# Performance work log

Measured on AMD Instinct MI355X. Metric: run time of the kernel, lower is better.

The kernel has to match this reference:

```python
import jax, jax.numpy as jnp
import numpy as np

BS, SEQ, DK = 4, 4096, 128

def setup_inputs() -> dict:
    key = jax.random.key(0)
    kq, kk, kv = jax.random.split(key, 3)
    q = jax.random.normal(kq, (BS, SEQ, DK), dtype=jnp.float32)
    k = jax.random.normal(kk, (BS, SEQ, DK), dtype=jnp.float32)
    v = jax.random.normal(kv, (BS, SEQ, DK), dtype=jnp.float32)
    return {"q": q, "k": k, "v": v}

def reference(q, k, v):
    d_k = q.shape[-1]
    # scores: [bs, s_q, s_k]
    scaled = jnp.einsum('bqd,bkd->bqk', q, k) / jnp.sqrt(jnp.asarray(d_k, q.dtype))
    # NOTE: original torch code applies softmax over dim=1 (query axis), faithfully reproduced here.
    attn = jax.nn.softmax(scaled, axis=1)
    return jnp.einsum('bqk,bkd->bqd', attn, v)
```

## Files before the change

### kernel.cpp

```cpp
#include <hip/hip_runtime.h>
#include <hip/hip_bf16.h>

#define BS  4
#define SEQ 4096
#define DK  128

#define C1_SCALE (1.4426950408889634f / 11.313708498984761f)

typedef __attribute__((ext_vector_type(8))) short bf16x8;
typedef __attribute__((ext_vector_type(4))) float f32x4;
typedef unsigned short ushort_t;

__device__ inline unsigned pk_bf16(float a, float b) {
    __hip_bfloat162 h = __float22bfloat162_rn(make_float2(a, b));
    union { __hip_bfloat162 h2; unsigned u; } cv;
    cv.h2 = h;
    return cv.u;
}

__device__ inline bf16x8 pk8(float4 a, float4 b) {
    union { bf16x8 v; unsigned u[4]; } r;
    r.u[0] = pk_bf16(a.x, a.y);
    r.u[1] = pk_bf16(a.z, a.w);
    r.u[2] = pk_bf16(b.x, b.y);
    r.u[3] = pk_bf16(b.z, b.w);
    return r.v;
}

__device__ inline void gld_lds16(const ushort_t* g, ushort_t* l) {
    __builtin_amdgcn_global_load_lds(
        (const __attribute__((address_space(1))) unsigned int*)g,
        (__attribute__((address_space(3))) unsigned int*)l,
        16, 0, 0);
}

__global__ __launch_bounds__(256) void cast_qk_sw(
    const float* __restrict__ Q, const float* __restrict__ K,
    ushort_t* __restrict__ Qb, ushort_t* __restrict__ Kb)
{
    const int g = blockIdx.x * 256 + threadIdx.x;
    const int q = g >> 4, ap = g & 15;
    const int a = ap ^ (q & 15);
    const float* src = Q + (size_t)q * DK + a * 8;
    float4 x = *(const float4*)src, y = *(const float4*)(src + 4);
    x.x *= C1_SCALE; x.y *= C1_SCALE; x.z *= C1_SCALE; x.w *= C1_SCALE;
    y.x *= C1_SCALE; y.y *= C1_SCALE; y.z *= C1_SCALE; y.w *= C1_SCALE;
    *(bf16x8*)(Qb + (size_t)g * 8) = pk8(x, y);
    src = K + (size_t)q * DK + a * 8;
    float4 x2 = *(const float4*)src, y2 = *(const float4*)(src + 4);
    *(bf16x8*)(Kb + (size_t)g * 8) = pk8(x2, y2);
}

__global__ __launch_bounds__(256) void sdpa_lsum(
    const ushort_t* __restrict__ Qb, const ushort_t* __restrict__ Kb,
    float* __restrict__ lp)
{
    __shared__ ushort_t Qs[2][4096];

    const int kt = blockIdx.x, qs = blockIdx.y, b = blockIdx.z;
    const int tid = threadIdx.x;
    const int w = tid >> 6, lane = tid & 63, ln = lane & 15, quad = lane >> 4;

    bf16x8 ka[2][4];
#pragma unroll
    for (int mt = 0; mt < 2; ++mt)
#pragma unroll
        for (int c = 0; c < 4; ++c)
            ka[mt][c] = *(const bf16x8*)(Kb +
                ((size_t)(b * SEQ) + kt * 128 + w * 32 + mt * 16 + ln) * DK +
                (((c * 4 + quad) ^ ln) * 8));

    float ls[2][4] = {};
    const ushort_t* qtb = Qb + ((size_t)(b * SEQ + qs * 512)) * DK;

#define A_DMA(BUF, I)                                                          \
    {                                                                          \
        _Pragma("unroll")                                                      \
        for (int j = 0; j < 2; ++j)                                            \
            gld_lds16(qtb + (size_t)(I) * 4096 + (j * 256 + tid) * 8,          \
                      &Qs[BUF][(j * 256 + w * 64) * 8]);                       \
    }

#define A_CMP(BUF)                                                             \
    {                                                                          \
        bf16x8 qf[2][4];                                                       \
        _Pragma("unroll")                                                      \
        for (int nt = 0; nt < 2; ++nt)                                         \
            _Pragma("unroll")                                                  \
            for (int c = 0; c < 4; ++c)                                        \
                qf[nt][c] = *(const bf16x8*)&Qs[BUF][(nt * 16 + ln) * 128 +    \
                                    (((c * 4 + quad) ^ ln) * 8)];              \
        _Pragma("unroll")                                                      \
        for (int mt = 0; mt < 2; ++mt)                                         \
            _Pragma("unroll")                                                  \
            for (int nt = 0; nt < 2; ++nt) {                                   \
                f32x4 s = {0.f, 0.f, 0.f, 0.f};                                \
                __builtin_amdgcn_s_setprio(1);                                 \
                _Pragma("unroll")                                              \
                for (int c = 0; c < 4; ++c)                                    \
                    s = __builtin_amdgcn_mfma_f32_16x16x32_bf16(               \
                        ka[mt][c], qf[nt][c], s, 0, 0, 0);                     \
                __builtin_amdgcn_s_setprio(0);                                 \
                _Pragma("unroll")                                              \
                for (int r = 0; r < 4; ++r)                                    \
                    ls[mt][r] += __builtin_amdgcn_exp2f(s[r]);                 \
            }                                                                  \
    }

    A_DMA(0, 0)
    for (int ii = 0; ii < 8; ++ii) {
        const int i0 = 2 * ii;
        __syncthreads();
        A_DMA(1, i0 + 1)
        A_CMP(0)
        __syncthreads();
        if (ii < 7) A_DMA(0, i0 + 2)
        A_CMP(1)
    }
#undef A_DMA
#undef A_CMP

#pragma unroll
    for (int mt = 0; mt < 2; ++mt)
#pragma unroll
        for (int r = 0; r < 4; ++r) {
            float vv = ls[mt][r];
            vv += __shfl_xor(vv, 1);
            vv += __shfl_xor(vv, 2);
            vv += __shfl_xor(vv, 4);
            vv += __shfl_xor(vv, 8);
            ls[mt][r] = vv;
        }
    if (ln < 8) {
        int k = kt * 128 + w * 32 + (ln >> 2) * 16 + quad * 4 + (ln & 3);
        lp[((size_t)(qs * BS + b)) * SEQ + k] = ls[ln >> 2][ln & 3];
    }
}

__global__ __launch_bounds__(256) void vb_transpose(
    const float* __restrict__ V, const float* __restrict__ lp,
    ushort_t* __restrict__ VbT)
{
    __shared__ float Vl[64][132];
    __shared__ float Wl[64];

    const int kt = blockIdx.x, b = blockIdx.y;
    const int tid = threadIdx.x;
    const int k0 = kt * 64;
    {
        int r = tid >> 2, sg = tid & 3;
        const float* src = V + ((size_t)(b * SEQ) + k0 + r) * DK + sg * 32;
#pragma unroll
        for (int i = 0; i < 8; ++i)
            *(float4*)&Vl[r][sg * 32 + i * 4] = *(const float4*)(src + i * 4);
    }
    if (tid < 64) {
        float s = 0.f;
#pragma unroll
        for (int qs = 0; qs < 8; ++qs)
            s += lp[((size_t)(qs * BS + b)) * SEQ + k0 + tid];
        Wl[tid] = 1.0f / s;
    }
    __syncthreads();

    const int d = tid >> 1, kh = tid & 1;
    unsigned u[16];
#pragma unroll
    for (int j = 0; j < 16; ++j) {
        int row = kh * 32 + j * 2;
        u[j] = pk_bf16(Vl[row][d] * Wl[row], Vl[row + 1][d] * Wl[row + 1]);
    }
    ushort_t* dst = VbT + ((size_t)(b * DK) + d) * SEQ + k0 + kh * 32;
#pragma unroll
    for (int i = 0; i < 4; ++i) {
        uint4 t4; t4.x = u[i*4]; t4.y = u[i*4+1]; t4.z = u[i*4+2]; t4.w = u[i*4+3];
        *(uint4*)(dst + i * 8) = t4;
    }
}

__global__ __launch_bounds__(256) void sdpa_out(
    const ushort_t* __restrict__ Qb, const ushort_t* __restrict__ Kb,
    const ushort_t* __restrict__ VbT,
    float* __restrict__ Op, float* __restrict__ O, int use_partial)
{
    __shared__ ushort_t Kt[2][8192];
    __shared__ ushort_t Vt[2][8192];
    __shared__ ushort_t Pt[4096];

    const int g  = blockIdx.x;
    const int qt = blockIdx.y;
    const int ks = g >> 2, b = g & 3;
    const int tid = threadIdx.x;
    const int w = tid >> 6, lane = tid & 63, ln = lane & 15, quad = lane >> 4;

    bf16x8 qa[4][4];
#pragma unroll
    for (int nt = 0; nt < 4; ++nt)
#pragma unroll
        for (int c = 0; c < 4; ++c)
            qa[c][nt] = *(const bf16x8*)(Qb +
                ((size_t)(b * SEQ) + qt * 64 + nt * 16 + ln) * DK +
                (((c * 4 + quad) ^ ln) * 8));

    f32x4 acc[4][2];
#pragma unroll
    for (int i = 0; i < 4; ++i)
#pragma unroll
        for (int j = 0; j < 2; ++j) acc[i][j] = (f32x4){0.f, 0.f, 0.f, 0.f};

    const ushort_t* ksrc = Kb + ((size_t)(b * SEQ) + ks * 1024) * DK;
    const ushort_t* vsrc = VbT + ((size_t)(b * DK)) * SEQ + ks * 1024;
    const int vd = tid >> 3, vap = tid & 7;

#define O_DMA(BUF, PH)                                                         \
    {                                                                          \
        _Pragma("unroll")                                                      \
        for (int j = 0; j < 4; ++j)                                            \
            gld_lds16(ksrc + (size_t)(PH) * 64 * DK + (j * 256 + tid) * 8,     \
                      &Kt[BUF][(j * 256 + w * 64) * 8]);                       \
        _Pragma("unroll")                                                      \
        for (int j = 0; j < 4; ++j)                                            \
            gld_lds16(vsrc + (size_t)(j * 32 + vd) * SEQ + (PH) * 64 +         \
                          ((vap ^ (vd & 7)) * 8),                              \
                      &Vt[BUF][(j * 256 + w * 64) * 8]);                       \
    }

#define QK_PHASE(BUF)                                                          \
    {                                                                          \
        bf16x8 kf[4];                                                          \
        _Pragma("unroll")                                                      \
        for (int c = 0; c < 4; ++c)                                            \
            kf[c] = *(const bf16x8*)&Kt[BUF][(w * 16 + ln) * 128 +             \
                                             (((c * 4 + quad) ^ ln) * 8)];     \
        _Pragma("unroll")                                                      \
        for (int nt = 0; nt < 4; ++nt) {                                       \
            f32x4 s = {0.f, 0.f, 0.f, 0.f};                                    \
            __builtin_amdgcn_s_setprio(1);                                     \
            _Pragma("unroll")                                                  \
            for (int c = 0; c < 4; ++c)                                        \
                s = __builtin_amdgcn_mfma_f32_16x16x32_bf16(kf[c], qa[c][nt], s, 0, 0, 0); \
            __builtin_amdgcn_s_setprio(0);                                     \
            uint2 pw;                                                          \
            pw.x = pk_bf16(__builtin_amdgcn_exp2f(s[0]),                       \
                           __builtin_amdgcn_exp2f(s[1]));                      \
            pw.y = pk_bf16(__builtin_amdgcn_exp2f(s[2]),                       \
                           __builtin_amdgcn_exp2f(s[3]));                      \
            const int q = nt * 16 + ln;                                        \
            const int a16 = w * 2 + (quad >> 1);                               \
            *(uint2*)&Pt[q * 64 + ((a16 ^ (q & 7)) * 8) + (quad & 1) * 4] = pw; \
        }                                                                      \
    }

#define PV_PHASE(BUF)                                                          \
    {                                                                          \
        _Pragma("unroll")                                                      \
        for (int kc = 0; kc < 2; ++kc) {                                       \
            bf16x8 pa[4], vfr[2];                                              \
            _Pragma("unroll")                                                  \
            for (int qf2 = 0; qf2 < 4; ++qf2)                                  \
                pa[qf2] = *(const bf16x8*)&Pt[(qf2 * 16 + ln) * 64 +           \
                                    (((kc * 4 + quad) ^ (ln & 7)) * 8)];       \
            _Pragma("unroll")                                                  \
            for (int dt = 0; dt < 2; ++dt)                                     \
                vfr[dt] = *(const bf16x8*)&Vt[BUF][(w * 32 + dt * 16 + ln) * 64 + \
                                    (((kc * 4 + quad) ^ (ln & 7)) * 8)];       \
            __builtin_amdgcn_s_setprio(1);                                     \
            _Pragma("unroll")                                                  \
            for (int qf2 = 0; qf2 < 4; ++qf2)                                  \
                _Pragma("unroll")                                              \
                for (int dt = 0; dt < 2; ++dt)                                 \
                    acc[qf2][dt] = __builtin_amdgcn_mfma_f32_16x16x32_bf16(    \
                        pa[qf2], vfr[dt], acc[qf2][dt], 0, 0, 0);              \
            __builtin_amdgcn_s_setprio(0);                                     \
        }                                                                      \
    }

    O_DMA(0, 0)
    for (int ph = 0; ph < 16; ++ph) {
        const int cur = ph & 1;
        __syncthreads();
        if (ph < 15) O_DMA(cur ^ 1, ph + 1)
        QK_PHASE(cur)
        __syncthreads();
        PV_PHASE(cur)
    }
#undef O_DMA
#undef QK_PHASE
#undef PV_PHASE

    if (use_partial) {
        float* dst = Op + (size_t)ks * ((size_t)BS * SEQ * DK) +
                     ((size_t)(b * SEQ) + qt * 64 + quad * 4) * DK + w * 32 + ln;
#pragma unroll
        for (int qf2 = 0; qf2 < 4; ++qf2)
#pragma unroll
            for (int dt = 0; dt < 2; ++dt)
#pragma unroll
                for (int r = 0; r < 4; ++r)
                    dst[((size_t)(qf2 * 16 + r)) * DK + dt * 16] = acc[qf2][dt][r];
    } else {
#pragma unroll
        for (int qf2 = 0; qf2 < 4; ++qf2)
#pragma unroll
            for (int dt = 0; dt < 2; ++dt)
#pragma unroll
                for (int r = 0; r < 4; ++r)
                    atomicAdd(&O[((size_t)(b * SEQ) + qt * 64 + qf2 * 16 + quad * 4 + r) * DK +
                                 w * 32 + dt * 16 + ln], acc[qf2][dt][r]);
    }
}

__global__ __launch_bounds__(256) void reduce4(
    const float* __restrict__ Op, float* __restrict__ O)
{
    const size_t N = (size_t)BS * SEQ * DK;
    size_t i = ((size_t)blockIdx.x * 256 + threadIdx.x) * 4;
    float4 a0 = *(const float4*)(Op + i);
    float4 a1 = *(const float4*)(Op + N + i);
    float4 a2 = *(const float4*)(Op + 2 * N + i);
    float4 a3 = *(const float4*)(Op + 3 * N + i);
    float4 r;
    r.x = a0.x + a1.x + a2.x + a3.x;
    r.y = a0.y + a1.y + a2.y + a3.y;
    r.z = a0.z + a1.z + a2.z + a3.z;
    r.w = a0.w + a1.w + a2.w + a3.w;
    *(float4*)(O + i) = r;
}

extern "C" void kernel_launch(void* const* d_in, const int* in_sizes, int n_in,
                              void* d_out, int out_size, void* d_ws, size_t ws_size,
                              hipStream_t stream) {
    const float* q = (const float*)d_in[0];
    const float* k = (const float*)d_in[1];
    const float* v = (const float*)d_in[2];
    float* out = (float*)d_out;

    const size_t QKV = (size_t)BS * SEQ * DK;
    float*    lp  = (float*)d_ws;
    ushort_t* Qb  = (ushort_t*)((char*)d_ws + (1 << 20));
    ushort_t* Kb  = Qb + QKV;
    ushort_t* VbT = Kb + QKV;
    float*    Op  = (float*)(VbT + QKV);

    const size_t need_p = (1u << 20) + 3 * QKV * 2 + 4 * QKV * sizeof(float);

    cast_qk_sw<<<dim3(BS * SEQ * 16 / 256), 256, 0, stream>>>(q, k, Qb, Kb);
    sdpa_lsum  <<<dim3(32, 8, 4), 256, 0, stream>>>(Qb, Kb, lp);
    vb_transpose<<<dim3(64, 4),   256, 0, stream>>>(v, lp, VbT);

    if (ws_size >= need_p) {
        sdpa_out<<<dim3(16, 64), 256, 0, stream>>>(Qb, Kb, VbT, Op, out, 1);
        reduce4 <<<dim3(BS * SEQ * DK / 4 / 256), 256, 0, stream>>>(Op, out);
    } else {
        hipMemsetAsync(out, 0, QKV * sizeof(float), stream);
        sdpa_out<<<dim3(16, 64), 256, 0, stream>>>(Qb, Kb, VbT, nullptr, out, 0);
    }
}
```

Before: 172.4 us.

## Deepen DMA prefetch pipelines with triple buffering and explicit waitcnt barriers

In the lsum kernel, the Q tile buffer goes from two slots to three so two tiles are in flight while one is consumed. Each iteration now waits on a partial vmcnt and one raw s_barrier instead of two __syncthreads. The output kernel also prefetches two tiles ahead, using explicit vmcnt/lgkmcnt waits and raw barriers, and issues the next DMA after the PV phase. The aim is to hide global-to-LDS load latency and cut full-drain synchronisation. The cost is more LDS, and correctness depends on the hand-counted waitcnt values matching the number of outstanding loads.

Measured after the change: 153.1 us. -11.2%, faster.

```diff
diff --git a/kernel.cpp b/kernel.cpp
--- a/kernel.cpp
+++ b/kernel.cpp
@@ -32,6 +32,11 @@
         (const __attribute__((address_space(1))) unsigned int*)g,
         (__attribute__((address_space(3))) unsigned int*)l,
         16, 0, 0);
+}
+
+__device__ inline void bar_fence() {
+    __builtin_amdgcn_s_barrier();
+    asm volatile("" ::: "memory");
 }
 
 __global__ __launch_bounds__(256) void cast_qk_sw(
@@ -55,7 +60,7 @@
     const ushort_t* __restrict__ Qb, const ushort_t* __restrict__ Kb,
     float* __restrict__ lp)
 {
-    __shared__ ushort_t Qs[2][4096];
+    __shared__ ushort_t Qs[3][4096];
 
     const int kt = blockIdx.x, qs = blockIdx.y, b = blockIdx.z;
     const int tid = threadIdx.x;
@@ -108,15 +113,16 @@
     }
 
     A_DMA(0, 0)
-    for (int ii = 0; ii < 8; ++ii) {
-        const int i0 = 2 * ii;
-        __syncthreads();
-        A_DMA(1, i0 + 1)
-        A_CMP(0)
-        __syncthreads();
-        if (ii < 7) A_DMA(0, i0 + 2)
-        A_CMP(1)
-    }
+    A_DMA(1, 1)
+    for (int t = 0; t < 15; ++t) {
+        asm volatile("s_waitcnt vmcnt(2) lgkmcnt(0)" ::: "memory");
+        bar_fence();
+        if (t < 14) A_DMA((t + 2) % 3, t + 2)
+        A_CMP(t % 3)
+    }
+    asm volatile("s_waitcnt vmcnt(0) lgkmcnt(0)" ::: "memory");
+    bar_fence();
+    A_CMP(0)
 #undef A_DMA
 #undef A_CMP
 
@@ -276,14 +282,25 @@
     }
 
     O_DMA(0, 0)
-    for (int ph = 0; ph < 16; ++ph) {
+    O_DMA(1, 1)
+    for (int ph = 0; ph < 15; ++ph) {
         const int cur = ph & 1;
-        __syncthreads();
-        if (ph < 15) O_DMA(cur ^ 1, ph + 1)
+        asm volatile("s_waitcnt vmcnt(8)" ::: "memory");
+        bar_fence();
         QK_PHASE(cur)
-        __syncthreads();
+        asm volatile("s_waitcnt lgkmcnt(0)" ::: "memory");
+        bar_fence();
         PV_PHASE(cur)
-    }
+        asm volatile("s_waitcnt lgkmcnt(0)" ::: "memory");
+        bar_fence();
+        if (ph < 14) O_DMA(cur, ph + 2)
+    }
+    asm volatile("s_waitcnt vmcnt(0)" ::: "memory");
+    bar_fence();
+    QK_PHASE(1)
+    asm volatile("s_waitcnt lgkmcnt(0)" ::: "memory");
+    bar_fence();
+    PV_PHASE(1)
 #undef O_DMA
 #undef QK_PHASE
 #undef PV_PHASE
```
